# Kernel optimization log

Hardware: AMD Instinct MI355X
Metric: run time of the kernel (lower is better)

The kernel has to match this reference:

```python
import jax, jax.numpy as jnp
import numpy as np
from jax import lax

C = 2  # channels, fixed by get_weight(2)

def _rep_pad(x):
    # ReplicationPad2d((0,1,0,1)): pad right and bottom by 1, edge-replicate
    return jnp.pad(x, ((0, 0), (0, 0), (0, 1), (0, 1)), mode='edge')

def _dwconv(x, w):
    # depthwise 2x2 valid conv; w has OIHW shape (C,1,2,2)
    return lax.conv_general_dilated(
        x, w, window_strides=(1, 1), padding='VALID',
        dimension_numbers=('NCHW', 'OIHW', 'NCHW'),
        feature_group_count=x.shape[1])

def _stencils():
    gx1 = np.array([[-1., 1.], [0., 0.]], np.float32)
    gx2 = np.array([[0., 0.], [-1., 1.]], np.float32)
    gy1 = np.array([[-1., 0.], [1., 0.]], np.float32)
    gy2 = np.array([[0., -1.], [0., 1.]], np.float32)
    mk = lambda k: jnp.asarray(np.tile(k[None, None], (C, 1, 1, 1)))
    return mk(gx1), mk(gx2), mk(gy1), mk(gy2)

def setup_inputs() -> dict:
    key = jax.random.key(0)
    k1, k2, k3, k4 = jax.random.split(key, 4)
    B, H, W = 16, 768, 768
    u = jax.random.normal(k1, (B, C, H, W), jnp.float32)
    a = jax.random.uniform(k2, (B, C, H + 2, W + 2), jnp.float32)
    b = jax.random.normal(k3, (B, C, H + 2, W + 2), jnp.float32)
    c = jax.random.uniform(k4, (B, C, H + 2, W + 2), jnp.float32)
    gx1, gx2, gy1, gy2 = _stencils()
    alpha = jnp.float32(0.49)
    tau = jnp.float32(1.0 / (4.0 * (1.0 - 0.49)))  # alpha>0 branch in __init__
    return {'u': u, 'a': a, 'b': b, 'c': c,
            'grad_x1': gx1, 'grad_x2': gx2, 'grad_y1': gy1, 'grad_y2': gy2,
            'alpha': alpha, 'tau': tau}

def reference(u, a, b, c, grad_x1, grad_x2, grad_y1, grad_y2, alpha, tau):
    a = a[:, :, 1:, 1:]
    b = b[:, :, 1:, 1:]
    c = c[:, :, 1:, 1:]
    sign = jnp.sign(b)
    beta = (1.0 - 2.0 * alpha) * sign
    w1a = a * (1 - alpha) / 2
    w2a = a * alpha / 2
    w1b = b * (1 - beta) / 4
    w2b = b * (1 + beta) / 4
    w1c = c * (1 - alpha) / 2
    w2c = c * alpha / 2
    pu = _rep_pad(u)
    ux1 = _rep_pad(_dwconv(pu, grad_x1))
    ux2 = _rep_pad(_dwconv(pu, grad_x2))
    uy1 = _rep_pad(_dwconv(pu, grad_y1))
    uy2 = _rep_pad(_dwconv(pu, grad_y2))
    flip = lambda w: -w[:, :, ::-1, ::-1]
    uxx1 = _dwconv(w1a * ux1 + w2a * ux2 + w1b * uy1 + w2b * uy2, flip(grad_x1))
    uxx2 = _dwconv(w2a * ux1 + w1a * ux2 + w2b * uy1 + w1b * uy2, flip(grad_x2))
    uyy1 = _dwconv(w1b * ux1 + w2b * ux2 + w1c * uy1 + w2c * uy2, flip(grad_y1))
    uyy2 = _dwconv(w2b * ux1 + w1b * ux2 + w2c * uy1 + w1c * uy2, flip(grad_y2))
    Au = 0.5 * (uxx1 + uxx2 + uyy1 + uyy2)
    return u + tau * Au
```

## Files before the change

### kernel.cpp

```cpp
#include <hip/hip_runtime.h>

#define HH 768
#define WW 768
#define HP 770
#define WP 770


typedef float f4 __attribute__((ext_vector_type(4)));

__device__ inline f4 ld4u(const float* p) {
    f4 v;
    __builtin_memcpy(&v, p, sizeof(f4));
    return v;
}

__global__ __launch_bounds__(256) void diffusion_kernel(
    const float* __restrict__ u,
    const float* __restrict__ a,
    const float* __restrict__ b,
    const float* __restrict__ c,
    const float* __restrict__ alpha_p,
    const float* __restrict__ tau_p,
    float* __restrict__ out)
{
    const int lane = threadIdx.x & 63;
    const int rsub = threadIdx.x >> 6;
    const int j0 = (blockIdx.x * 64 + lane) * 4;
    const int i0 = blockIdx.y * 8 + rsub * 2;
    const int bc = blockIdx.z;

    const float alpha = *alpha_p;
    const float tau   = *tau_p;
    const float c1 = (1.0f - alpha) * 0.5f;
    const float c2 = alpha * 0.5f;
    const float g  = 1.0f - 2.0f * alpha;

    const float* __restrict__ ub = u + (size_t)bc * (HH * WW);
    const float* __restrict__ ab = a + (size_t)bc * (HP * WP);
    const float* __restrict__ bb = b + (size_t)bc * (HP * WP);
    const float* __restrict__ cb = c + (size_t)bc * (HP * WP);

    int ur[4];
    ur[0] = i0; ur[1] = i0 + 1;
    ur[2] = min(i0 + 2, HH - 1); ur[3] = min(i0 + 3, HH - 1);

    float U[4][6];
    const bool interior = (j0 + 7 < WW);
#pragma unroll
    for (int rr = 0; rr < 4; ++rr) {
        const float* pr = ub + (size_t)ur[rr] * WW + j0;
        f4 t = *(const f4*)pr;
        U[rr][0] = t.x; U[rr][1] = t.y; U[rr][2] = t.z; U[rr][3] = t.w;
        if (interior) {
            f4 s = *(const f4*)(pr + 4);
            U[rr][4] = s.x; U[rr][5] = s.y;
        } else {
            U[rr][4] = t.w; U[rr][5] = t.w;
        }
    }

    float A[3][5], B[3][5], C[3][5];
#pragma unroll
    for (int k = 0; k < 3; ++k) {
        const size_t roff = (size_t)(i0 + 1 + k) * WP + (j0 + 1);
        f4 t;
        t = ld4u(ab + roff); A[k][0]=t.x; A[k][1]=t.y; A[k][2]=t.z; A[k][3]=t.w; A[k][4]=ab[roff+4];
        t = ld4u(bb + roff); B[k][0]=t.x; B[k][1]=t.y; B[k][2]=t.z; B[k][3]=t.w; B[k][4]=bb[roff+4];
        t = ld4u(cb + roff); C[k][0]=t.x; C[k][1]=t.y; C[k][2]=t.z; C[k][3]=t.w; C[k][4]=cb[roff+4];
    }

    auto wts = [&](float Av, float Bv, float Cv,
                   float& w1a, float& w2a, float& w1b, float& w2b,
                   float& w1c, float& w2c) {
        w1a = Av * c1; w2a = Av * c2;
        const float gb = g * fabsf(Bv);
        w1b = (Bv - gb) * 0.25f; w2b = (Bv + gb) * 0.25f;
        w1c = Cv * c1; w2c = Cv * c2;
    };

#pragma unroll
    for (int r = 0; r < 2; ++r) {
        float res[4];
#pragma unroll
        for (int p = 0; p < 4; ++p) {
            float acc = 0.0f;
            float w1a, w2a, w1b, w2b, w1c, w2c;
            float ux1, ux2, uy1, uy2;

            wts(A[r][p], B[r][p], C[r][p], w1a, w2a, w1b, w2b, w1c, w2c);
            ux1 = U[r][p+1]   - U[r][p];     ux2 = U[r+1][p+1] - U[r+1][p];
            uy1 = U[r+1][p]   - U[r][p];     uy2 = U[r+1][p+1] - U[r][p+1];
            acc -= (w2a + w2b) * ux1 + (w1a + w1b) * ux2
                 + (w2b + w2c) * uy1 + (w1b + w1c) * uy2;

            wts(A[r][p+1], B[r][p+1], C[r][p+1], w1a, w2a, w1b, w2b, w1c, w2c);
            ux1 = U[r][p+2]   - U[r][p+1];   ux2 = U[r+1][p+2] - U[r+1][p+1];
            uy1 = U[r+1][p+1] - U[r][p+1];   uy2 = U[r+1][p+2] - U[r][p+2];
            acc += (w2a - w1b) * ux1 + (w1a - w2b) * ux2
                 + (w2b - w1c) * uy1 + (w1b - w2c) * uy2;

            wts(A[r+1][p], B[r+1][p], C[r+1][p], w1a, w2a, w1b, w2b, w1c, w2c);
            ux1 = U[r+1][p+1] - U[r+1][p];   ux2 = U[r+2][p+1] - U[r+2][p];
            uy1 = U[r+2][p]   - U[r+1][p];   uy2 = U[r+2][p+1] - U[r+1][p+1];
            acc += (w2b - w1a) * ux1 + (w1b - w2a) * ux2
                 + (w2c - w1b) * uy1 + (w1c - w2b) * uy2;

            wts(A[r+1][p+1], B[r+1][p+1], C[r+1][p+1], w1a, w2a, w1b, w2b, w1c, w2c);
            ux1 = U[r+1][p+2] - U[r+1][p+1]; ux2 = U[r+2][p+2] - U[r+2][p+1];
            uy1 = U[r+2][p+1] - U[r+1][p+1]; uy2 = U[r+2][p+2] - U[r+1][p+2];
            acc += (w1a + w1b) * ux1 + (w2a + w2b) * ux2
                 + (w1b + w1c) * uy1 + (w2b + w2c) * uy2;

            res[p] = U[r][p] + tau * 0.5f * acc;
        }

        f4 o;
        o.x = res[0]; o.y = res[1]; o.z = res[2]; o.w = res[3];
        __builtin_nontemporal_store(
            o, (f4*)(out + (size_t)bc * (HH * WW) + (size_t)(i0 + r) * WW + j0));
    }
}

extern "C" void kernel_launch(void* const* d_in, const int* in_sizes, int n_in,
                              void* d_out, int out_size, void* d_ws, size_t ws_size,
                              hipStream_t stream) {
    const float* u     = (const float*)d_in[0];
    const float* a     = (const float*)d_in[1];
    const float* b     = (const float*)d_in[2];
    const float* c     = (const float*)d_in[3];
    const float* alpha = (const float*)d_in[8];
    const float* tau   = (const float*)d_in[9];
    float* out = (float*)d_out;

    dim3 block(256, 1, 1);
    dim3 grid(WW / 256, HH / 8, 32);
    diffusion_kernel<<<grid, block, 0, stream>>>(u, a, b, c, alpha, tau, out);
}
```

Measured before the change: 82.53 us.

## Stream 8 rows per thread with rolling register window and prefetch

Each thread now computes a 4-wide by 8-row strip, keeping a sliding three-row window of u and a two-row window of a/b/c in registers, and prefetches the next row while computing the current one. This removes the redundant halo-row loads of the old 2-rows-per-thread scheme. The grid is flattened into a 1D launch with an XCD-aware block remap, so consecutive tiles land on the same chiplet. It trades fewer threads and more serial work per thread for less memory traffic, which may reduce latency hiding.

```diff
diff --git a/kernel.cpp b/kernel.cpp
--- a/kernel.cpp
+++ b/kernel.cpp
@@ -4,6 +4,9 @@
 #define WW 768
 #define HP 770
 #define WP 770
+#define ROWS 8
+#define TILES 192
+#define BANDS 96
 
 
 typedef float f4 __attribute__((ext_vector_type(4)));
@@ -23,11 +26,14 @@
     const float* __restrict__ tau_p,
     float* __restrict__ out)
 {
-    const int lane = threadIdx.x & 63;
-    const int rsub = threadIdx.x >> 6;
-    const int j0 = (blockIdx.x * 64 + lane) * 4;
-    const int i0 = blockIdx.y * 8 + rsub * 2;
-    const int bc = blockIdx.z;
+    const int bid  = (blockIdx.x & 7) * (TILES * BANDS * 32 / 256 / 8) + (blockIdx.x >> 3);
+    const int gtid = bid * 256 + threadIdx.x;
+    const int tile = gtid % TILES;
+    const int band = (gtid / TILES) % BANDS;
+    const int bc   = gtid / (TILES * BANDS);
+    const int j0 = tile * 4;
+    const int i0 = band * ROWS;
+    const bool interior = (j0 + 4) < WW;
 
     const float alpha = *alpha_p;
     const float tau   = *tau_p;
@@ -39,35 +45,33 @@
     const float* __restrict__ ab = a + (size_t)bc * (HP * WP);
     const float* __restrict__ bb = b + (size_t)bc * (HP * WP);
     const float* __restrict__ cb = c + (size_t)bc * (HP * WP);
+    float* __restrict__ outb = out + (size_t)bc * (HH * WW);
 
-    int ur[4];
-    ur[0] = i0; ur[1] = i0 + 1;
-    ur[2] = min(i0 + 2, HH - 1); ur[3] = min(i0 + 3, HH - 1);
+    float u0[6], u1[6], u2[6];
+    float a1[5], a2[5], b1[5], b2[5], cc1[5], cc2[5];
 
-    float U[4][6];
-    const bool interior = (j0 + 7 < WW);
-#pragma unroll
-    for (int rr = 0; rr < 4; ++rr) {
-        const float* pr = ub + (size_t)ur[rr] * WW + j0;
-        f4 t = *(const f4*)pr;
-        U[rr][0] = t.x; U[rr][1] = t.y; U[rr][2] = t.z; U[rr][3] = t.w;
-        if (interior) {
-            f4 s = *(const f4*)(pr + 4);
-            U[rr][4] = s.x; U[rr][5] = s.y;
-        } else {
-            U[rr][4] = t.w; U[rr][5] = t.w;
-        }
-    }
+    auto load_u = [&](int row, float* dst) {
+        const float* pr = ub + (size_t)row * WW + j0;
+        f4 t0 = *(const f4*)pr;
+        const float* p2 = pr + (interior ? 4 : 0);
+        f4 t1 = *(const f4*)p2;
+        dst[0] = t0.x; dst[1] = t0.y; dst[2] = t0.z; dst[3] = t0.w;
+        dst[4] = interior ? t1.x : t0.w;
+        dst[5] = interior ? t1.y : t0.w;
+    };
+    auto load_w = [&](const float* base, int row, float* dst) {
+        const float* pr = base + (size_t)row * WP + (j0 + 1);
+        f4 t = ld4u(pr);
+        dst[0] = t.x; dst[1] = t.y; dst[2] = t.z; dst[3] = t.w;
+        dst[4] = pr[4];
+    };
 
-    float A[3][5], B[3][5], C[3][5];
-#pragma unroll
-    for (int k = 0; k < 3; ++k) {
-        const size_t roff = (size_t)(i0 + 1 + k) * WP + (j0 + 1);
-        f4 t;
-        t = ld4u(ab + roff); A[k][0]=t.x; A[k][1]=t.y; A[k][2]=t.z; A[k][3]=t.w; A[k][4]=ab[roff+4];
-        t = ld4u(bb + roff); B[k][0]=t.x; B[k][1]=t.y; B[k][2]=t.z; B[k][3]=t.w; B[k][4]=bb[roff+4];
-        t = ld4u(cb + roff); C[k][0]=t.x; C[k][1]=t.y; C[k][2]=t.z; C[k][3]=t.w; C[k][4]=cb[roff+4];
-    }
+    load_u(i0,     u0);
+    load_u(i0 + 1, u1);
+    load_u(i0 + 2, u2);
+    load_w(ab, i0 + 1, a1);  load_w(ab, i0 + 2, a2);
+    load_w(bb, i0 + 1, b1);  load_w(bb, i0 + 2, b2);
+    load_w(cb, i0 + 1, cc1); load_w(cb, i0 + 2, cc2);
 
     auto wts = [&](float Av, float Bv, float Cv,
                    float& w1a, float& w2a, float& w1b, float& w2b,
@@ -79,7 +83,17 @@
     };
 
 #pragma unroll
-    for (int r = 0; r < 2; ++r) {
+    for (int r = 0; r < ROWS; ++r) {
+        const int ri = i0 + r;
+
+        float pu[6], pa[5], pb[5], pc[5];
+        if (r < ROWS - 1) {
+            load_u(min(ri + 3, HH - 1), pu);
+            load_w(ab, ri + 3, pa);
+            load_w(bb, ri + 3, pb);
+            load_w(cb, ri + 3, pc);
+        }
+
         float res[4];
 #pragma unroll
         for (int p = 0; p < 4; ++p) {
@@ -87,37 +101,47 @@
             float w1a, w2a, w1b, w2b, w1c, w2c;
             float ux1, ux2, uy1, uy2;
 
-            wts(A[r][p], B[r][p], C[r][p], w1a, w2a, w1b, w2b, w1c, w2c);
-            ux1 = U[r][p+1]   - U[r][p];     ux2 = U[r+1][p+1] - U[r+1][p];
-            uy1 = U[r+1][p]   - U[r][p];     uy2 = U[r+1][p+1] - U[r][p+1];
+            wts(a1[p], b1[p], cc1[p], w1a, w2a, w1b, w2b, w1c, w2c);
+            ux1 = u0[p+1] - u0[p];   ux2 = u1[p+1] - u1[p];
+            uy1 = u1[p]   - u0[p];   uy2 = u1[p+1] - u0[p+1];
             acc -= (w2a + w2b) * ux1 + (w1a + w1b) * ux2
                  + (w2b + w2c) * uy1 + (w1b + w1c) * uy2;
 
-            wts(A[r][p+1], B[r][p+1], C[r][p+1], w1a, w2a, w1b, w2b, w1c, w2c);
-            ux1 = U[r][p+2]   - U[r][p+1];   ux2 = U[r+1][p+2] - U[r+1][p+1];
-            uy1 = U[r+1][p+1] - U[r][p+1];   uy2 = U[r+1][p+2] - U[r][p+2];
+            wts(a1[p+1], b1[p+1], cc1[p+1], w1a, w2a, w1b, w2b, w1c, w2c);
+            ux1 = u0[p+2] - u0[p+1]; ux2 = u1[p+2] - u1[p+1];
+            uy1 = u1[p+1] - u0[p+1]; uy2 = u1[p+2] - u0[p+2];
             acc += (w2a - w1b) * ux1 + (w1a - w2b) * ux2
                  + (w2b - w1c) * uy1 + (w1b - w2c) * uy2;
 
-            wts(A[r+1][p], B[r+1][p], C[r+1][p], w1a, w2a, w1b, w2b, w1c, w2c);
-            ux1 = U[r+1][p+1] - U[r+1][p];   ux2 = U[r+2][p+1] - U[r+2][p];
-            uy1 = U[r+2][p]   - U[r+1][p];   uy2 = U[r+2][p+1] - U[r+1][p+1];
+            wts(a2[p], b2[p], cc2[p], w1a, w2a, w1b, w2b, w1c, w2c);
+            ux1 = u1[p+1] - u1[p];   ux2 = u2[p+1] - u2[p];
+            uy1 = u2[p]   - u1[p];   uy2 = u2[p+1] - u1[p+1];
             acc += (w2b - w1a) * ux1 + (w1b - w2a) * ux2
                  + (w2c - w1b) * uy1 + (w1c - w2b) * uy2;
 
-            wts(A[r+1][p+1], B[r+1][p+1], C[r+1][p+1], w1a, w2a, w1b, w2b, w1c, w2c);
-            ux1 = U[r+1][p+2] - U[r+1][p+1]; ux2 = U[r+2][p+2] - U[r+2][p+1];
-            uy1 = U[r+2][p+1] - U[r+1][p+1]; uy2 = U[r+2][p+2] - U[r+1][p+2];
+            wts(a2[p+1], b2[p+1], cc2[p+1], w1a, w2a, w1b, w2b, w1c, w2c);
+            ux1 = u1[p+2] - u1[p+1]; ux2 = u2[p+2] - u2[p+1];
+            uy1 = u2[p+1] - u1[p+1]; uy2 = u2[p+2] - u1[p+2];
             acc += (w1a + w1b) * ux1 + (w2a + w2b) * ux2
                  + (w1b + w1c) * uy1 + (w2b + w2c) * uy2;
 
-            res[p] = U[r][p] + tau * 0.5f * acc;
+            res[p] = u0[p] + tau * 0.5f * acc;
         }
 
         f4 o;
         o.x = res[0]; o.y = res[1]; o.z = res[2]; o.w = res[3];
-        __builtin_nontemporal_store(
-            o, (f4*)(out + (size_t)bc * (HH * WW) + (size_t)(i0 + r) * WW + j0));
+        __builtin_nontemporal_store(o, (f4*)(outb + (size_t)ri * WW + j0));
+
+        if (r < ROWS - 1) {
+#pragma unroll
+            for (int q = 0; q < 6; ++q) { u0[q] = u1[q]; u1[q] = u2[q]; u2[q] = pu[q]; }
+#pragma unroll
+            for (int q = 0; q < 5; ++q) {
+                a1[q] = a2[q];  a2[q] = pa[q];
+                b1[q] = b2[q];  b2[q] = pb[q];
+                cc1[q] = cc2[q]; cc2[q] = pc[q];
+            }
+        }
     }
 }
 
@@ -133,6 +157,6 @@
     float* out = (float*)d_out;
 
     dim3 block(256, 1, 1);
-    dim3 grid(WW / 256, HH / 8, 32);
+    dim3 grid(TILES * BANDS * 32 / 256, 1, 1);
     diffusion_kernel<<<grid, block, 0, stream>>>(u, a, b, c, alpha, tau, out);
 }
```

Result: faster. 68.28 us (-17.3%).
